# Kernel tuning notes

Hardware: AMD Instinct MI355X
Metric: run time of the kernel (lower is better)

Reference implementation:

```python
import jax, jax.numpy as jnp
import numpy as np
from jax.scipy.special import erf

F = 64          # scalar feature channels (hidden_irreps multiplicity)
S = 9           # spherical harmonics dim for max_ell=2
NB = 8          # num_bessel
RMAX = 5.0
PPOLY = 5       # num_polynomial_cutoff
AVG_NEIGH = 16.0
SIGMA = 1.0     # atomic_multipoles_smearing_width
KE = 1.0        # Coulomb constant (model units)
N = 20000; G = 20; E = 320000; NEL = 10; L = 2; HMLP = 16

def _sph_l2(u):
    # real spherical harmonics up to l=2, e3nn 'component' normalization,
    # with permute_to_e3nn_convention (y, z, x) ordering for l=1
    x, y, z = u[..., 0], u[..., 1], u[..., 2]
    s3 = 1.7320508075688772; s5 = 2.23606797749979; s15 = 3.872983346207417
    return jnp.stack([jnp.ones_like(x),
                      s3 * y, s3 * z, s3 * x,
                      s15 * x * y, s15 * y * z, 0.5 * s5 * (3.0 * z * z - 1.0),
                      s15 * x * z, 0.5 * s15 * (x * x - y * y)], axis=-1)

def _radial(r):
    # Bessel basis with smooth polynomial cutoff (p = PPOLY)
    n = jnp.arange(1, NB + 1, dtype=r.dtype)
    rb = jnp.sqrt(2.0 / RMAX) * jnp.sin(n * jnp.pi * r[:, None] / RMAX) / r[:, None]
    x = r / RMAX
    p = float(PPOLY)
    u = (1.0 - 0.5 * (p + 1.0) * (p + 2.0) * x**PPOLY
         + p * (p + 2.0) * x**(PPOLY + 1) - 0.5 * p * (p + 1.0) * x**(PPOLY + 2))
    u = jnp.where(x < 1.0, u, 0.0)
    return rb * u[:, None]

def setup_inputs() -> dict:
    key = jax.random.key(0)
    ks = jax.random.split(key, 20)
    Ng = N // G
    species = jax.random.randint(ks[0], (N,), 0, NEL)
    node_attrs = jax.nn.one_hot(species, NEL, dtype=jnp.float32)
    positions = jax.random.uniform(ks[1], (N, 3), dtype=jnp.float32) * 10.0
    g = jax.random.randint(ks[2], (E,), 0, G)
    s_loc = jax.random.randint(ks[3], (E,), 0, Ng)
    off = jax.random.randint(ks[4], (E,), 1, Ng)   # avoid self edges
    r_loc = (s_loc + off) % Ng
    edge_index = jnp.stack([g * Ng + s_loc, g * Ng + r_loc], axis=0)
    batch = jnp.repeat(jnp.arange(G), Ng)
    sc = 0.1
    atomic_energies = jax.random.normal(ks[5], (NEL,)) * sc
    embed_w = jax.random.normal(ks[6], (NEL, F)) * sc
    radial_w1 = jax.random.normal(ks[7], (L, NB, 64)) * 0.3
    radial_b1 = jnp.zeros((L, 64), jnp.float32)
    radial_w2 = jax.random.normal(ks[8], (L, 64, F)) * 0.2
    prod_w = jax.random.normal(ks[9], (L, NEL, F)) * 0.3
    readout_w = jax.random.normal(ks[10], (L, F)) * sc
    ro2_w1 = jax.random.normal(ks[11], (F, HMLP)) * 0.2
    ro2_b1 = jnp.zeros((HMLP,), jnp.float32)
    ro2_w2 = jax.random.normal(ks[12], (HMLP, 1)) * 0.2
    charge_w = jax.random.normal(ks[13], (L, F)) * sc
    flux_w = jax.random.normal(ks[14], (L, NB)) * sc
    formal_charges = jax.random.normal(ks[15], (NEL,)) * 0.5
    return dict(node_attrs=node_attrs, positions=positions, edge_index=edge_index,
                batch=batch, num_graphs=G, atomic_energies=atomic_energies,
                embed_w=embed_w, radial_w1=radial_w1, radial_b1=radial_b1,
                radial_w2=radial_w2, prod_w=prod_w, readout_w=readout_w,
                ro2_w1=ro2_w1, ro2_b1=ro2_b1, ro2_w2=ro2_w2,
                charge_w=charge_w, flux_w=flux_w, formal_charges=formal_charges)

def reference(node_attrs, positions, edge_index, batch, num_graphs,
              atomic_energies, embed_w, radial_w1, radial_b1, radial_w2,
              prod_w, readout_w, ro2_w1, ro2_b1, ro2_w2,
              charge_w, flux_w, formal_charges):
    Nn = node_attrs.shape[0]
    Ng = Nn // num_graphs
    snd, rcv = edge_index[0], edge_index[1]
    # atomic reference energies (E0) and node embedding
    node_e0 = node_attrs @ atomic_energies                      # [N]
    e0 = jax.ops.segment_sum(node_e0, batch, num_graphs)        # [G]
    node_scalars = node_attrs @ embed_w                         # [N,F]
    # edge geometry: gather, spherical harmonics, radial embedding
    vec = positions[rcv] - positions[snd]                       # [E,3]
    lengths = jnp.sqrt((vec * vec).sum(-1) + 1e-12)             # [E]
    unit = vec / lengths[:, None]
    edge_attrs = _sph_l2(unit)                                  # [E,S]
    edge_feats = _radial(lengths)                               # [E,NB]
    # formal charges (per-species)
    FQ = node_attrs @ formal_charges                            # [N]
    charge_density = FQ
    flux = jnp.zeros_like(lengths)
    energies = [e0]
    node_e_list = [node_e0]
    nL = radial_w1.shape[0]
    for l in range(nL):
        # interaction: radial MLP -> per-edge TP messages -> scatter sum
        R = jax.nn.silu(edge_feats @ radial_w1[l] + radial_b1[l]) @ radial_w2[l]  # [E,F]
        m = (R * node_scalars[snd])[:, :, None] * edge_attrs[:, None, :]          # [E,F,S]
        agg = jax.ops.segment_sum(m, rcv, Nn) / AVG_NEIGH                         # [N,F,S]
        # equivariant product (correlation-2 flavor) + element-dependent skip
        sk = node_scalars * (node_attrs @ prod_w[l])                              # [N,F]
        feats = agg + agg * agg[:, :, :1]                                         # [N,F,S]
        node_scalars = feats[:, :, 0] + sk                                        # [N,F]
        if l == nL - 1:
            node_energies = (jax.nn.silu(node_scalars @ ro2_w1 + ro2_b1) @ ro2_w2)[:, 0]
        else:
            node_energies = node_scalars @ readout_w[l]
        energies.append(jax.ops.segment_sum(node_energies, batch, num_graphs))
        node_e_list.append(node_energies)
        # long-range source maps: per-node charge + per-edge flux contributions
        charge_density = charge_density + node_scalars @ charge_w[l]
        flux = flux + edge_feats @ flux_w[l]
    contributions = jnp.stack(energies, -1)                     # [G, L+1]
    total_energy = contributions.sum(-1)                        # [G]
    node_energy = jnp.stack(node_e_list, -1).sum(-1)            # [N]
    # polarization: edge-flux dipole + formal-charge dipole
    pol = jax.ops.segment_sum(flux[:, None] * vec, batch[rcv], num_graphs)
    pol = pol + jax.ops.segment_sum(FQ[:, None] * positions, batch, num_graphs)
    # direct (non-PBC) screened Coulomb energy per graph, equal-size graphs
    q = charge_density.reshape(num_graphs, Ng)
    p = positions.reshape(num_graphs, Ng, 3)
    d = p[:, :, None, :] - p[:, None, :, :]
    r = jnp.sqrt((d * d).sum(-1) + 1e-12)
    kern = erf(r / (2.0 * SIGMA)) / r * (1.0 - jnp.eye(Ng, dtype=r.dtype))
    e_el = 0.5 * KE * jnp.einsum('gi,gij,gj->g', q, kern, q)
    total_energy = total_energy + e_el
    total_charge = jax.ops.segment_sum(charge_density, batch, num_graphs)
    return total_energy, node_energy, contributions, pol, total_charge
```

## Files before the change

kernel.cpp:

```cpp
#include <hip/hip_runtime.h>
#include <math.h>

#define NEL 10
#define FD 64
#define NBES 8
#define GG 20
#define HML 16
#define EGB 1280
#define NUB 5000
#define TKNOT 2048
#define TROWS 2049
#define TBBLK 1025

__device__ __forceinline__ float wred(float v) {
    #pragma unroll
    for (int off = 32; off > 0; off >>= 1) v += __shfl_down(v, off, 64);
    return v;
}

__device__ __forceinline__ float silu(float h) {
    return h / (1.f + __expf(-h));
}

__device__ __forceinline__ int xcd_swizzle(int bid, int nb) {
    int q = nb >> 3, r = nb & 7;
    int x = bid & 7, i = bid >> 3;
    return (x < r ? x * (q + 1) : r * (q + 1) + (x - r) * q) + i;
}

__global__ __launch_bounds__(256) void hist_k(
    const int* __restrict__ eidx, int* __restrict__ cnt, int E_)
{
    int e = blockIdx.x * 256 + threadIdx.x;
    atomicAdd(&cnt[eidx[E_ + e]], 1);
}

__global__ __launch_bounds__(1024) void scan_k(
    const int* __restrict__ cnt, int* __restrict__ cur, int N_)
{
    int t = threadIdx.x;
    __shared__ int wtot[16];
    int lane = t & 63, wid = t >> 6;
    int base = t * 20;
    int c[20]; int s = 0;
    bool full = (base + 20 <= N_);
    if (full) {
        #pragma unroll
        for (int i = 0; i < 5; ++i) {
            int4 v4 = *(const int4*)&cnt[base + i * 4];
            c[i*4+0] = v4.x; c[i*4+1] = v4.y; c[i*4+2] = v4.z; c[i*4+3] = v4.w;
        }
        #pragma unroll
        for (int i = 0; i < 20; ++i) s += c[i];
    } else {
        #pragma unroll
        for (int i = 0; i < 20; ++i) { int idx = base + i; c[i] = (idx < N_) ? cnt[idx] : 0; s += c[i]; }
    }
    int v = s;
    #pragma unroll
    for (int off = 1; off < 64; off <<= 1) {
        int u = __shfl_up(v, off, 64);
        if (lane >= off) v += u;
    }
    if (lane == 63) wtot[wid] = v;
    __syncthreads();
    if (wid == 0 && lane < 16) {
        int wv = wtot[lane];
        #pragma unroll
        for (int off = 1; off < 16; off <<= 1) {
            int u = __shfl_up(wv, off, 64);
            if (lane >= off) wv += u;
        }
        wtot[lane] = wv;
    }
    __syncthreads();
    int ex = (wid > 0 ? wtot[wid - 1] : 0) + (v - s);
    if (full) {
        int o[20];
        #pragma unroll
        for (int i = 0; i < 20; ++i) { o[i] = ex; ex += c[i]; }
        #pragma unroll
        for (int i = 0; i < 5; ++i)
            *(int4*)&cur[base + i * 4] = make_int4(o[i*4+0], o[i*4+1], o[i*4+2], o[i*4+3]);
    } else {
        #pragma unroll
        for (int i = 0; i < 20; ++i) {
            int idx = base + i;
            if (idx < N_) { cur[idx] = ex; ex += c[i]; }
        }
    }
}

__global__ __launch_bounds__(256) void setup_geom_k(
    const float* __restrict__ pos, const int* __restrict__ eidx,
    const float* __restrict__ flux_w, int* __restrict__ cur,
    uint2* __restrict__ recs, float* __restrict__ polpart,
    const float* __restrict__ attrs, const float* __restrict__ ae,
    const float* __restrict__ fc, const float* __restrict__ embed_w,
    int* __restrict__ spec, float* __restrict__ q, float* __restrict__ out,
    float* __restrict__ scal,
    const float* __restrict__ w1, const float* __restrict__ b1,
    const float* __restrict__ w2, float* __restrict__ tab,
    int N_, int E_, int ng)
{
    int bid = blockIdx.x, t = threadIdx.x;
    const float PI = 3.14159265358979323846f;
    if (bid < EGB) {
        __shared__ float lpol[GG * 3];
        for (int i = t; i < GG * 3; i += 256) lpol[i] = 0.f;
        __syncthreads();
        int e = bid * 256 + t;
        if (e < E_) {
            float fw[NBES];
            #pragma unroll
            for (int i = 0; i < NBES; ++i) fw[i] = flux_w[i] + flux_w[NBES + i];
            unsigned int magic = (unsigned int)(0xFFFFFFFFull / (unsigned int)ng) + 1u;
            int s = eidx[e], r = eidx[E_ + e];
            float dx = pos[(size_t)r*3+0] - pos[(size_t)s*3+0];
            float dy = pos[(size_t)r*3+1] - pos[(size_t)s*3+1];
            float dz = pos[(size_t)r*3+2] - pos[(size_t)s*3+2];
            float len = sqrtf(dx*dx + dy*dy + dz*dz + 1e-12f);
            float x = len * 0.2f;
            float u = 0.f;
            if (x < 1.f) {
                float x2 = x * x;
                float x5 = x2 * x2 * x;
                u = 1.f - 21.f * x5 + 35.f * x5 * x - 15.f * x5 * x2;
            }
            float pref = 0.6324555320336759f / len * u;
            float theta = PI * x;
            float s1, c1;
            __sincosf(theta, &s1, &c1);
            float c2 = 2.f * c1;
            float sp_ = 0.f, sn = s1;
            float flux = 0.f;
            #pragma unroll
            for (int i = 0; i < NBES; ++i) {
                flux += pref * sn * fw[i];
                float n1 = c2 * sn - sp_; sp_ = sn; sn = n1;
            }
            int p = atomicAdd(&cur[r], 1);
            recs[p] = make_uint2((unsigned int)s | ((unsigned int)r << 16),
                                 __float_as_uint(len));
            int g = (int)__umulhi((unsigned int)r, magic);
            atomicAdd(&lpol[g*3+0], flux * dx);
            atomicAdd(&lpol[g*3+1], flux * dy);
            atomicAdd(&lpol[g*3+2], flux * dz);
        }
        __syncthreads();
        for (int i = t; i < GG * 3; i += 256) polpart[bid * (GG * 3) + i] = lpol[i];
    } else if (bid < EGB + TBBLK) {
        if (bid == EGB && t < GG) out[t] = 0.f;
        int widg = (bid - EGB) * 4 + (t >> 6);
        if (widg < 2 * TROWS) {
            int l = widg / TROWS;
            int kk = widg - l * TROWS;
            int f = t & 63;
            float len = fmaxf((float)kk * (5.f / (float)TKNOT), 1e-6f);
            float x = len * 0.2f;
            float u = 0.f;
            if (x < 1.f) {
                float x2 = x * x;
                float x5 = x2 * x2 * x;
                u = 1.f - 21.f * x5 + 35.f * x5 * x - 15.f * x5 * x2;
            }
            float pref = 0.6324555320336759f / len * u;
            float theta = PI * x;
            float s1, c1;
            __sincosf(theta, &s1, &c1);
            float c2 = 2.f * c1;
            float sp_ = 0.f, sn = s1;
            float ef[NBES];
            #pragma unroll
            for (int i = 0; i < NBES; ++i) {
                ef[i] = pref * sn;
                float n1 = c2 * sn - sp_; sp_ = sn; sn = n1;
            }
            float h = b1[l * FD + f];
            #pragma unroll
            for (int j = 0; j < NBES; ++j)
                h = fmaf(ef[j], w1[l * 512 + j * 64 + f], h);
            h = silu(h);
            float o = 0.f;
            #pragma unroll
            for (int m = 0; m < 64; ++m)
                o = fmaf(__shfl(h, m, 64), w2[(size_t)l * 4096 + m * 64 + f], o);
            float* tbase = tab + (size_t)l * TKNOT * 64 * 2;
            if (kk < TKNOT) tbase[((size_t)kk * 64 + f) * 2 + 0] = o;
            if (kk > 0)     tbase[((size_t)(kk - 1) * 64 + f) * 2 + 1] = o;
        }
    } else {
        int idx = (bid - (EGB + TBBLK)) * 256 + t;
        int lane = t & 63;
        int n = idx >> 6;
        bool pred = (lane < NEL) && (attrs[(size_t)n * NEL + lane] > 0.5f);
        unsigned long long m = __ballot(pred);
        int sp = (int)__builtin_ctzll(m);
        scal[idx] = embed_w[sp * FD + lane];
        if (lane == 0) { spec[n] = sp; q[n] = fc[sp]; out[GG + n] = ae[sp]; }
    }
}

__global__ __launch_bounds__(256, 4) void edge_node_k(
    const uint2* __restrict__ recs, const float* __restrict__ tab,
    const int* __restrict__ cur,
    const float* __restrict__ scal_in, float* __restrict__ scal_out,
    const int* __restrict__ spec, const float* __restrict__ prod_w,
    const float* __restrict__ readout_w, const float* __restrict__ ro2_w1,
    const float* __restrict__ ro2_b1, const float* __restrict__ ro2_w2,
    const float* __restrict__ charge_w, float* __restrict__ q,
    float* __restrict__ out_nodeE, float* __restrict__ nEpart,
    int layer, int last, int N_)
{
    __shared__ float vsh[4][FD];
    int t = threadIdx.x, w = t >> 6, lane = t & 63;
    int xb = xcd_swizzle(blockIdx.x, gridDim.x);
    int W = xb * 4 + w;
    int r0 = W * 4;
    int e0 = (r0 == 0) ? 0 : cur[r0 - 1];
    int e1 = cur[r0 + 3];
    const float* tb = tab + (size_t)layer * TKNOT * 64 * 2;

    float a0 = 0.f, a1 = 0.f, a2 = 0.f, a3 = 0.f;
    int curR = r0; float run = 0.f;

    for (int base = e0; base < e1; base += 64) {
        int nn = e1 - base; if (nn > 64) nn = 64;
        uint2 rec;
        if (base + lane < e1) rec = recs[base + lane];
        else rec = make_uint2((unsigned int)(r0 + 3) << 16, 0u);
        float ln = __uint_as_float(rec.y);
        float ttf = ln * ((float)TKNOT / 5.f);
        int k0 = (int)ttf; k0 = max(0, min(k0, TKNOT - 1));
        float frl = fminf(fmaxf(ttf - (float)k0, 0.f), 1.f);
        int offl = k0 * 128;

        #pragma unroll 1
        for (int sub = 0; sub < 4; ++sub) {
            int sb = sub * 16;
            if (sb >= nn) break;
            unsigned int idv[16]; int offk[16]; float frk[16];
            #pragma unroll
            for (int k = 0; k < 16; ++k) {
                int pp = sb + k;
                idv[k] = __builtin_amdgcn_readlane(rec.x, pp);
                offk[k] = __builtin_amdgcn_readlane(offl, pp);
                frk[k] = __uint_as_float((unsigned int)__builtin_amdgcn_readlane(
                             __float_as_uint(frl), pp));
            }
            float2 rab[16]; float sw[16];
            #pragma unroll
            for (int k = 0; k < 16; ++k) {
                rab[k] = *(const float2*)&tb[(size_t)offk[k] + lane * 2];
                sw[k]  = scal_in[(size_t)(idv[k] & 0xffffu) * FD + lane];
            }
            #pragma unroll
            for (int k = 0; k < 16; ++k) {
                int r = (int)(idv[k] >> 16);
                float R = fmaf(frk[k], rab[k].y - rab[k].x, rab[k].x);
                float v = ((sb + k) < nn) ? R * sw[k] : 0.f;
                if (r != curR) {
                    int ri = curR - r0;
                    if (ri == 0) a0 = run; else if (ri == 1) a1 = run;
                    else if (ri == 2) a2 = run; else a3 = run;
                    curR = r; run = v;
                } else {
                    run += v;
                }
            }
        }
    }
    {
        int ri = curR - r0;
        if (ri == 0) a0 = run; else if (ri == 1) a1 = run;
        else if (ri == 2) a2 = run; else a3 = run;
    }

    float neAcc = 0.f;
    #pragma unroll
    for (int i = 0; i < 4; ++i) {
        float acc = (i == 0) ? a0 : (i == 1) ? a1 : (i == 2) ? a2 : a3;
        int rr = r0 + i;
        float a = acc * 0.0625f;
        int sp = spec[rr];
        size_t idx = (size_t)rr * FD + lane;
        float v = a + a * a + scal_in[idx] * prod_w[(layer * NEL + sp) * FD + lane];
        if (!last) scal_out[idx] = v;
        float ne;
        if (!last) {
            ne = wred(v * readout_w[layer * FD + lane]);
        } else {
            vsh[w][lane] = v;
            int l16 = lane & 15, qq = lane >> 4;
            float hp = 0.f;
            #pragma unroll
            for (int ff = 0; ff < 16; ++ff) {
                int fidx = qq * 16 + ff;
                hp += vsh[w][fidx] * ro2_w1[fidx * HML + l16];
            }
            hp += __shfl_down(hp, 32, 64);
            hp += __shfl_down(hp, 16, 64);
            float h = 0.f;
            if (lane < HML) h = silu(ro2_b1[lane] + hp) * ro2_w2[lane];
            ne = wred(h);
        }
        float qs = wred(v * charge_w[layer * FD + lane]);
        if (lane == 0) {
            out_nodeE[rr] += ne;
            q[rr] += qs;
            neAcc += ne;
        }
    }
    if (lane == 0) nEpart[layer * NUB + W] = neAcc;
}

__global__ __launch_bounds__(256) void coulomb_final_k(
    const float* __restrict__ q, const float* __restrict__ pos,
    const int* __restrict__ spec, const float* __restrict__ ae,
    const float* __restrict__ fc, const float* __restrict__ nEpart,
    const float* __restrict__ polpart, float* __restrict__ out,
    int N_, int ng)
{
    __shared__ float sh[260];
    int vb = blockIdx.x;
    int g = vb / 137, rem = vb % 137;
    int t = threadIdx.x, lane = t & 63, w = t >> 6;

    if (rem < 136) {
        int a = 0, r2 = rem;
        while (r2 >= 16 - a) { r2 -= 16 - a; ++a; }
        int b = a + r2;
        const float* qg = q + (size_t)g * ng;
        const float* pg = pos + (size_t)g * ng * 3;
        float* qs_ = sh; float* jx = sh + 64; float* jy = sh + 128; float* jz = sh + 192;
        if (t < 64) {
            int j = b * 64 + t;
            bool ok = j < ng;
            qs_[t] = ok ? qg[j] : 0.f;
            jx[t] = ok ? pg[(size_t)j*3+0] : 0.f;
            jy[t] = ok ? pg[(size_t)j*3+1] : 0.f;
            jz[t] = ok ? pg[(size_t)j*3+2] : 0.f;
        }
        __syncthreads();
        int i = a * 64 + lane;
        float accu = 0.f;
        if (i < ng) {
            float qi = qg[i];
            float xi = pg[(size_t)i*3+0], yi = pg[(size_t)i*3+1], zi = pg[(size_t)i*3+2];
            #pragma unroll 4
            for (int k = 0; k < 16; ++k) {
                int jj = w * 16 + k;
                int j = b * 64 + jj;
                float dx = xi - jx[jj], dy = yi - jy[jj], dz = zi - jz[jj];
                float d2 = dx*dx + dy*dy + dz*dz + 1e-12f;
                float rinv = __frsqrt_rn(d2);
                float r = d2 * rinv;
                float x = 0.5f * r;
                float tt = __frcp_rn(1.f + 0.3275911f * x);
                float poly = ((((1.061405429f*tt - 1.453152027f)*tt + 1.421413741f)*tt
                               - 0.284496736f)*tt + 0.254829592f)*tt;
                float erfv = 1.f - poly * __expf(-x * x);
                float kern = (j == i) ? 0.f : erfv * rinv;
                accu += qi * qs_[jj] * kern;
            }
        }
        accu = wred(accu);
        if (lane == 0) sh[256 + w] = accu;
        __syncthreads();
        if (t == 0) {
            float s = sh[256] + sh[257] + sh[258] + sh[259];
            atomicAdd(&out[g], (a == b) ? 0.5f * s : s);
        }
    } else {
        float se0 = 0.f, sq = 0.f, p0 = 0.f, p1 = 0.f, p2 = 0.f, s0 = 0.f, s1 = 0.f;
        for (int n = g * ng + t; n < (g + 1) * ng; n += 256) {
            int sp = spec[n];
            float fq = fc[sp];
            se0 += ae[sp];
            sq += q[n];
            p0 += fq * pos[(size_t)n*3+0];
            p1 += fq * pos[(size_t)n*3+1];
            p2 += fq * pos[(size_t)n*3+2];
        }
        if (t < 250) {
            int b = g * 250 + t;
            s0 = nEpart[b];
            s1 = nEpart[NUB + b];
        }
        for (int b = t; b < EGB; b += 256) {
            p0 += polpart[b * (GG * 3) + g * 3 + 0];
            p1 += polpart[b * (GG * 3) + g * 3 + 1];
            p2 += polpart[b * (GG * 3) + g * 3 + 2];
        }
        float vals[7] = {se0, s0, s1, sq, p0, p1, p2};
        float* red = sh;
        #pragma unroll
        for (int k = 0; k < 7; ++k) {
            float r = wred(vals[k]);
            if (lane == 0) red[w * 8 + k] = r;
        }
        __syncthreads();
        if (t < 7) sh[64 + t] = red[t] + red[8 + t] + red[16 + t] + red[24 + t];
        __syncthreads();
        if (t == 0) {
            float a0 = sh[64], a1 = sh[65], a2 = sh[66];
            atomicAdd(&out[g], a0 + a1 + a2);
            float* contrib = out + GG + N_;
            contrib[g*3+0] = a0; contrib[g*3+1] = a1; contrib[g*3+2] = a2;
            float* pol = contrib + GG * 3;
            pol[g*3+0] = sh[68]; pol[g*3+1] = sh[69]; pol[g*3+2] = sh[70];
            float* qt = pol + GG * 3;
            qt[g] = sh[67];
        }
    }
}

extern "C" void kernel_launch(void* const* d_in, const int* in_sizes, int n_in,
                              void* d_out, int out_size, void* d_ws, size_t ws_size,
                              hipStream_t stream)
{
    const float* node_attrs      = (const float*)d_in[0];
    const float* positions       = (const float*)d_in[1];
    const int*   edge_index      = (const int*)d_in[2];
    const float* atomic_energies = (const float*)d_in[5];
    const float* embed_w         = (const float*)d_in[6];
    const float* radial_w1       = (const float*)d_in[7];
    const float* radial_b1       = (const float*)d_in[8];
    const float* radial_w2       = (const float*)d_in[9];
    const float* prod_w          = (const float*)d_in[10];
    const float* readout_w       = (const float*)d_in[11];
    const float* ro2_w1          = (const float*)d_in[12];
    const float* ro2_b1          = (const float*)d_in[13];
    const float* ro2_w2          = (const float*)d_in[14];
    const float* charge_w        = (const float*)d_in[15];
    const float* flux_w          = (const float*)d_in[16];
    const float* formal_charges  = (const float*)d_in[17];

    int N = in_sizes[0] / NEL;
    int E = in_sizes[2] / 2;
    int ng = N / GG;

    float* ws      = (float*)d_ws;
    float* scal_a  = ws;
    float* scal_b  = scal_a + (size_t)N * FD;
    int*   cnt     = (int*)(scal_b + (size_t)N * FD);
    int*   cur     = cnt + N;
    uint2* recs    = (uint2*)(cur + N);
    float* q       = (float*)(recs + E);
    int*   spec    = (int*)(q + N);
    float* nEpart  = (float*)(spec + N);
    float* polpart = nEpart + 2 * NUB;
    float* tab     = polpart + EGB * (GG * 3);

    float* out = (float*)d_out;
    float* out_nodeE = out + GG;

    hipMemsetAsync(cnt, 0, (size_t)N * sizeof(int), stream);

    hist_k<<<E / 256, 256, 0, stream>>>(edge_index, cnt, E);
    scan_k<<<1, 1024, 0, stream>>>(cnt, cur, N);
    setup_geom_k<<<EGB + TBBLK + (N * FD) / 256, 256, 0, stream>>>(
        positions, edge_index, flux_w, cur, recs, polpart,
        node_attrs, atomic_energies, formal_charges, embed_w,
        spec, q, out, scal_a, radial_w1, radial_b1, radial_w2, tab, N, E, ng);

    edge_node_k<<<N / 16, 256, 0, stream>>>(
        recs, tab, cur, scal_a, scal_b, spec, prod_w, readout_w,
        ro2_w1, ro2_b1, ro2_w2, charge_w, q, out_nodeE, nEpart, 0, 0, N);
    edge_node_k<<<N / 16, 256, 0, stream>>>(
        recs, tab, cur, scal_b, scal_a, spec, prod_w, readout_w,
        ro2_w1, ro2_b1, ro2_w2, charge_w, q, out_nodeE, nEpart, 1, 1, N);

    coulomb_final_k<<<GG * 137, 256, 0, stream>>>(
        q, positions, spec, atomic_energies, formal_charges,
        nEpart, polpart, out, N, ng);
}
```

Measured before the change: 228.4 us.

## Assign one receiver node per wavefront in edge_node kernel

Each wavefront now handles one receiver node instead of four, so the grid grows fourfold and the per-edge receiver-change tracking with its four-way register select goes away. Per-node energies are written to an N-sized partial buffer, and the final kernel sums them in its existing per-node loop. This gives more parallelism and simpler inner-loop control flow, at the cost of more wavefronts with short edge lists (about 16 edges per node), leaving many lanes idle per 64-edge chunk and adding more per-node epilogue reductions.

```diff
diff --git a/kernel.cpp b/kernel.cpp
--- a/kernel.cpp
+++ b/kernel.cpp
@@ -7,7 +7,6 @@
 #define GG 20
 #define HML 16
 #define EGB 1280
-#define NUB 5000
 #define TKNOT 2048
 #define TROWS 2049
 #define TBBLK 1025
@@ -215,20 +214,18 @@
     __shared__ float vsh[4][FD];
     int t = threadIdx.x, w = t >> 6, lane = t & 63;
     int xb = xcd_swizzle(blockIdx.x, gridDim.x);
-    int W = xb * 4 + w;
-    int r0 = W * 4;
-    int e0 = (r0 == 0) ? 0 : cur[r0 - 1];
-    int e1 = cur[r0 + 3];
+    int rr = xb * 4 + w;
+    int e0 = (rr == 0) ? 0 : cur[rr - 1];
+    int e1 = cur[rr];
     const float* tb = tab + (size_t)layer * TKNOT * 64 * 2;
 
-    float a0 = 0.f, a1 = 0.f, a2 = 0.f, a3 = 0.f;
-    int curR = r0; float run = 0.f;
+    float run = 0.f;
 
     for (int base = e0; base < e1; base += 64) {
         int nn = e1 - base; if (nn > 64) nn = 64;
         uint2 rec;
         if (base + lane < e1) rec = recs[base + lane];
-        else rec = make_uint2((unsigned int)(r0 + 3) << 16, 0u);
+        else rec = make_uint2(0u, 0u);
         float ln = __uint_as_float(rec.y);
         float ttf = ln * ((float)TKNOT / 5.f);
         int k0 = (int)ttf; k0 = max(0, min(k0, TKNOT - 1));
@@ -236,9 +233,8 @@
         int offl = k0 * 128;
 
         #pragma unroll 1
-        for (int sub = 0; sub < 4; ++sub) {
+        for (int sub = 0; sub < 4 && sub * 16 < nn; ++sub) {
             int sb = sub * 16;
-            if (sb >= nn) break;
             unsigned int idv[16]; int offk[16]; float frk[16];
             #pragma unroll
             for (int k = 0; k < 16; ++k) {
@@ -256,62 +252,41 @@
             }
             #pragma unroll
             for (int k = 0; k < 16; ++k) {
-                int r = (int)(idv[k] >> 16);
                 float R = fmaf(frk[k], rab[k].y - rab[k].x, rab[k].x);
-                float v = ((sb + k) < nn) ? R * sw[k] : 0.f;
-                if (r != curR) {
-                    int ri = curR - r0;
-                    if (ri == 0) a0 = run; else if (ri == 1) a1 = run;
-                    else if (ri == 2) a2 = run; else a3 = run;
-                    curR = r; run = v;
-                } else {
-                    run += v;
-                }
-            }
-        }
-    }
-    {
-        int ri = curR - r0;
-        if (ri == 0) a0 = run; else if (ri == 1) a1 = run;
-        else if (ri == 2) a2 = run; else a3 = run;
-    }
-
-    float neAcc = 0.f;
-    #pragma unroll
-    for (int i = 0; i < 4; ++i) {
-        float acc = (i == 0) ? a0 : (i == 1) ? a1 : (i == 2) ? a2 : a3;
-        int rr = r0 + i;
-        float a = acc * 0.0625f;
-        int sp = spec[rr];
-        size_t idx = (size_t)rr * FD + lane;
-        float v = a + a * a + scal_in[idx] * prod_w[(layer * NEL + sp) * FD + lane];
-        if (!last) scal_out[idx] = v;
-        float ne;
-        if (!last) {
-            ne = wred(v * readout_w[layer * FD + lane]);
-        } else {
-            vsh[w][lane] = v;
-            int l16 = lane & 15, qq = lane >> 4;
-            float hp = 0.f;
-            #pragma unroll
-            for (int ff = 0; ff < 16; ++ff) {
-                int fidx = qq * 16 + ff;
-                hp += vsh[w][fidx] * ro2_w1[fidx * HML + l16];
-            }
-            hp += __shfl_down(hp, 32, 64);
-            hp += __shfl_down(hp, 16, 64);
-            float h = 0.f;
-            if (lane < HML) h = silu(ro2_b1[lane] + hp) * ro2_w2[lane];
-            ne = wred(h);
-        }
-        float qs = wred(v * charge_w[layer * FD + lane]);
-        if (lane == 0) {
-            out_nodeE[rr] += ne;
-            q[rr] += qs;
-            neAcc += ne;
-        }
-    }
-    if (lane == 0) nEpart[layer * NUB + W] = neAcc;
+                run += ((sb + k) < nn) ? R * sw[k] : 0.f;
+            }
+        }
+    }
+
+    float a = run * 0.0625f;
+    int sp = spec[rr];
+    size_t idx = (size_t)rr * FD + lane;
+    float v = a + a * a + scal_in[idx] * prod_w[(layer * NEL + sp) * FD + lane];
+    if (!last) scal_out[idx] = v;
+    float ne;
+    if (!last) {
+        ne = wred(v * readout_w[layer * FD + lane]);
+    } else {
+        vsh[w][lane] = v;
+        int l16 = lane & 15, qq = lane >> 4;
+        float hp = 0.f;
+        #pragma unroll
+        for (int ff = 0; ff < 16; ++ff) {
+            int fidx = qq * 16 + ff;
+            hp += vsh[w][fidx] * ro2_w1[fidx * HML + l16];
+        }
+        hp += __shfl_down(hp, 32, 64);
+        hp += __shfl_down(hp, 16, 64);
+        float h = 0.f;
+        if (lane < HML) h = silu(ro2_b1[lane] + hp) * ro2_w2[lane];
+        ne = wred(h);
+    }
+    float qs = wred(v * charge_w[layer * FD + lane]);
+    if (lane == 0) {
+        out_nodeE[rr] += ne;
+        q[rr] += qs;
+        nEpart[(size_t)layer * N_ + rr] = ne;
+    }
 }
 
 __global__ __launch_bounds__(256) void coulomb_final_k(
@@ -381,11 +356,8 @@
             p0 += fq * pos[(size_t)n*3+0];
             p1 += fq * pos[(size_t)n*3+1];
             p2 += fq * pos[(size_t)n*3+2];
-        }
-        if (t < 250) {
-            int b = g * 250 + t;
-            s0 = nEpart[b];
-            s1 = nEpart[NUB + b];
+            s0 += nEpart[n];
+            s1 += nEpart[(size_t)N_ + n];
         }
         for (int b = t; b < EGB; b += 256) {
             p0 += polpart[b * (GG * 3) + g * 3 + 0];
@@ -449,7 +421,7 @@
     float* q       = (float*)(recs + E);
     int*   spec    = (int*)(q + N);
     float* nEpart  = (float*)(spec + N);
-    float* polpart = nEpart + 2 * NUB;
+    float* polpart = nEpart + 2 * (size_t)N;
     float* tab     = polpart + EGB * (GG * 3);
 
     float* out = (float*)d_out;
@@ -464,10 +436,10 @@
         node_attrs, atomic_energies, formal_charges, embed_w,
         spec, q, out, scal_a, radial_w1, radial_b1, radial_w2, tab, N, E, ng);
 
-    edge_node_k<<<N / 16, 256, 0, stream>>>(
+    edge_node_k<<<N / 4, 256, 0, stream>>>(
         recs, tab, cur, scal_a, scal_b, spec, prod_w, readout_w,
         ro2_w1, ro2_b1, ro2_w2, charge_w, q, out_nodeE, nEpart, 0, 0, N);
-    edge_node_k<<<N / 16, 256, 0, stream>>>(
+    edge_node_k<<<N / 4, 256, 0, stream>>>(
         recs, tab, cur, scal_b, scal_a, spec, prod_w, readout_w,
         ro2_w1, ro2_b1, ro2_w2, charge_w, q, out_nodeE, nEpart, 1, 1, N);
 
```

New measurement: 227.8 us. About the same (-0.3%).
